# Kernel tuning notes

Measured on AMD Instinct MI355X. Metric: run time of the kernel, lower is better.

## Reference

```python
import jax, jax.numpy as jnp
import numpy as np


def setup_inputs() -> dict:
    key = jax.random.key(0)
    k_xyz, k_w1, k_b1, k_w2, k_b2 = jax.random.split(key, 5)
    B, N = 2, 1024
    D_MODEL, N_HEADS = 128, 8
    HID = D_MODEL // 2
    # Kaiming-ish init scale for the tiny MLP weights
    return {
        "xyz": jax.random.normal(k_xyz, (B, 3, N), dtype=jnp.float32),
        "W1": jax.random.normal(k_w1, (3, HID), dtype=jnp.float32) * (1.0 / np.sqrt(3.0)),
        "b1": jax.random.normal(k_b1, (HID,), dtype=jnp.float32) * 0.01,
        "W2": jax.random.normal(k_w2, (HID, N_HEADS), dtype=jnp.float32) * (1.0 / np.sqrt(HID)),
        "b2": jax.random.normal(k_b2, (N_HEADS,), dtype=jnp.float32) * 0.01,
    }


def reference(xyz, W1, b1, W2, b2):
    # xyz: [B, 3, N] -> [B, N, 3]
    pts = jnp.transpose(xyz, (0, 2, 1))
    # pairwise relative positions: rel[b, i, j, :] = pts[b, j] - pts[b, i]
    # (matches xyz.unsqueeze(1) - xyz.unsqueeze(2) in torch)
    rel = pts[:, None, :, :] - pts[:, :, None, :]          # [B, N, N, 3]
    h = jax.nn.relu(jnp.einsum("bijc,ch->bijh", rel, W1) + b1)  # [B, N, N, HID]
    bias = jnp.einsum("bijh,hk->bijk", h, W2) + b2         # [B, N, N, H]
    # permute(0, 3, 1, 2) -> [B, H, N, N]
    return jnp.transpose(bias, (0, 3, 1, 2))
```

## Files before the change

### kernel.cpp

```cpp
#include <hip/hip_runtime.h>
#include <hip/hip_bf16.h>

#define HID   64
#define NHD   8
#define IT    16
#define WAVES 8
#define JTW   32
#define JT    (WAVES*JTW)

typedef __attribute__((ext_vector_type(8))) short bf16x8;
typedef __attribute__((ext_vector_type(4))) float f32x4;

static __device__ __forceinline__ short f2bf(float f) {
  __hip_bfloat16 h = __float2bfloat16(f);
  short s; __builtin_memcpy(&s, &h, sizeof(s));
  return s;
}

__global__ __launch_bounds__(WAVES * 64, 4) void relposenc_mfma(
    const float* __restrict__ xyz, const float* __restrict__ W1,
    const float* __restrict__ b1,  const float* __restrict__ W2,
    const float* __restrict__ b2,  float* __restrict__ out, int N) {

  __shared__ float sW1b1[4][HID];
  __shared__ float sU[IT][HID];

  const int tid  = threadIdx.x;
  const int wave = tid >> 6;
  const int lane = tid & 63;
  const int col  = lane & 15;
  const int hgrp = lane >> 4;
  const int b    = blockIdx.z;
  const int i0   = blockIdx.y * IT;
  const int j0   = blockIdx.x * JT + wave * JTW;

  const float* xb = xyz + (size_t)b * 3 * N;

  if (tid < 4 * HID) {
    int r = tid >> 6, h = tid & 63;
    sW1b1[r][h] = (r < 3) ? W1[r * HID + h] : b1[h];
  }
  for (int t = tid; t < IT * HID; t += WAVES * 64) {
    int ii = t >> 6, h = t & 63;
    int i  = i0 + ii;
    sU[ii][h] = fmaf(xb[i], W1[h],
                fmaf(xb[N + i], W1[HID + h],
                     xb[2 * N + i] * W1[2 * HID + h]));
  }

  bf16x8 afrag[2];
  #pragma unroll
  for (int kb = 0; kb < 2; ++kb)
    #pragma unroll
    for (int e = 0; e < 8; ++e) {
      int h = kb * 32 + hgrp * 8 + e;
      float w = (col < NHD) ? W2[h * NHD + col] : 0.f;
      afrag[kb][e] = f2bf(w);
    }
  float b2v[4];
  #pragma unroll
  for (int r = 0; r < 4; ++r) b2v[r] = b2[(hgrp * 4 + r) & 7];

  __syncthreads();

  float aj[2][2][8];
  #pragma unroll
  for (int t = 0; t < 2; ++t) {
    int j = j0 + t * 16 + col;
    float x0 = xb[j], x1 = xb[N + j], x2 = xb[2 * N + j];
    #pragma unroll
    for (int kb = 0; kb < 2; ++kb)
      #pragma unroll
      for (int e = 0; e < 8; ++e) {
        int h = kb * 32 + hgrp * 8 + e;
        aj[t][kb][e] = fmaf(x0, sW1b1[0][h],
                       fmaf(x1, sW1b1[1][h],
                       fmaf(x2, sW1b1[2][h], sW1b1[3][h])));
      }
  }

  for (int ii = 0; ii < IT; ++ii) {
    const float4* pu = (const float4*)(&sU[ii][0]);
    float4 u0 = pu[hgrp * 2], u1 = pu[hgrp * 2 + 1];
    float4 u2 = pu[8 + hgrp * 2], u3 = pu[8 + hgrp * 2 + 1];
    float ui[2][8] = {{u0.x,u0.y,u0.z,u0.w, u1.x,u1.y,u1.z,u1.w},
                      {u2.x,u2.y,u2.z,u2.w, u3.x,u3.y,u3.z,u3.w}};
    const int i = i0 + ii;

    #pragma unroll
    for (int t = 0; t < 2; ++t) {
      f32x4 c = {0.f, 0.f, 0.f, 0.f};
      #pragma unroll
      for (int kb = 0; kb < 2; ++kb) {
        bf16x8 bf;
        #pragma unroll
        for (int e = 0; e < 8; ++e) {
          float v = aj[t][kb][e] - ui[kb][e];
          bf[e] = f2bf(v > 0.f ? v : 0.f);
        }
        c = __builtin_amdgcn_mfma_f32_16x16x32_bf16(afrag[kb], bf, c, 0, 0, 0);
      }
      if (lane < 32) {
        size_t jj = (size_t)j0 + t * 16 + col;
        #pragma unroll
        for (int r = 0; r < 4; ++r) {
          int k = hgrp * 4 + r;
          out[(((size_t)(b * NHD + k)) * N + i) * N + jj] = c[r] + b2v[r];
        }
      }
    }
  }
}

extern "C" void kernel_launch(void* const* d_in, const int* in_sizes, int n_in,
                              void* d_out, int out_size, void* d_ws, size_t ws_size,
                              hipStream_t stream) {
  const float* xyz = (const float*)d_in[0];
  const float* W1  = (const float*)d_in[1];
  const float* b1  = (const float*)d_in[2];
  const float* W2  = (const float*)d_in[3];
  const float* b2  = (const float*)d_in[4];
  float* out = (float*)d_out;

  const long long in0 = in_sizes[0];
  const int N = (int)((3LL * (long long)out_size) / (8LL * in0));
  const int B = (int)(in0 / (3LL * N));

  dim3 grid(N / JT, N / IT, B);
  relposenc_mfma<<<grid, WAVES * 64, 0, stream>>>(xyz, W1, b1, W2, b2, out, N);
}
```

Before: 24.31 us.

## Pack two j-tiles into one MFMA accumulator and use nontemporal stores

```diff
diff --git a/kernel.cpp b/kernel.cpp
--- a/kernel.cpp
+++ b/kernel.cpp
@@ -17,7 +17,7 @@
   return s;
 }
 
-__global__ __launch_bounds__(WAVES * 64, 4) void relposenc_mfma(
+__global__ __launch_bounds__(WAVES * 64, 4) void relposenc_mfma3(
     const float* __restrict__ xyz, const float* __restrict__ W1,
     const float* __restrict__ b1,  const float* __restrict__ W2,
     const float* __restrict__ b2,  float* __restrict__ out, int N) {
@@ -48,18 +48,18 @@
                      xb[2 * N + i] * W1[2 * HID + h]));
   }
 
-  bf16x8 afrag[2];
+  bf16x8 aLo[2], aHi[2];
   #pragma unroll
   for (int kb = 0; kb < 2; ++kb)
     #pragma unroll
     for (int e = 0; e < 8; ++e) {
       int h = kb * 32 + hgrp * 8 + e;
-      float w = (col < NHD) ? W2[h * NHD + col] : 0.f;
-      afrag[kb][e] = f2bf(w);
+      aLo[kb][e] = f2bf((col < NHD)  ? W2[h * NHD + col]        : 0.f);
+      aHi[kb][e] = f2bf((col >= NHD) ? W2[h * NHD + (col - 8)]  : 0.f);
     }
   float b2v[4];
   #pragma unroll
-  for (int r = 0; r < 4; ++r) b2v[r] = b2[(hgrp * 4 + r) & 7];
+  for (int r = 0; r < 4; ++r) b2v[r] = b2[((hgrp & 1) << 2) + r];
 
   __syncthreads();
 
@@ -79,35 +79,46 @@
       }
   }
 
+  const size_t jj = (size_t)j0 + col + ((size_t)(lane >> 5) << 4);
+  const int kbase = (hgrp & 1) << 2;
+  float* outp = out + ((size_t)(b * NHD + kbase) * N) * N + jj;
+  const size_t planeStride = (size_t)N * N;
+
+  const float4* pu = (const float4*)(&sU[0][0]);
+  float4 nu0 = pu[hgrp * 2],     nu1 = pu[hgrp * 2 + 1];
+  float4 nu2 = pu[8 + hgrp * 2], nu3 = pu[8 + hgrp * 2 + 1];
+
   for (int ii = 0; ii < IT; ++ii) {
-    const float4* pu = (const float4*)(&sU[ii][0]);
-    float4 u0 = pu[hgrp * 2], u1 = pu[hgrp * 2 + 1];
-    float4 u2 = pu[8 + hgrp * 2], u3 = pu[8 + hgrp * 2 + 1];
+    float4 u0 = nu0, u1 = nu1, u2 = nu2, u3 = nu3;
+    if (ii + 1 < IT) {
+      const float4* pn = (const float4*)(&sU[ii + 1][0]);
+      nu0 = pn[hgrp * 2];     nu1 = pn[hgrp * 2 + 1];
+      nu2 = pn[8 + hgrp * 2]; nu3 = pn[8 + hgrp * 2 + 1];
+    }
     float ui[2][8] = {{u0.x,u0.y,u0.z,u0.w, u1.x,u1.y,u1.z,u1.w},
                       {u2.x,u2.y,u2.z,u2.w, u3.x,u3.y,u3.z,u3.w}};
-    const int i = i0 + ii;
 
+    bf16x8 bf[2][2];
     #pragma unroll
-    for (int t = 0; t < 2; ++t) {
-      f32x4 c = {0.f, 0.f, 0.f, 0.f};
+    for (int t = 0; t < 2; ++t)
       #pragma unroll
-      for (int kb = 0; kb < 2; ++kb) {
-        bf16x8 bf;
+      for (int kb = 0; kb < 2; ++kb)
         #pragma unroll
         for (int e = 0; e < 8; ++e) {
           float v = aj[t][kb][e] - ui[kb][e];
-          bf[e] = f2bf(v > 0.f ? v : 0.f);
+          bf[t][kb][e] = f2bf(v > 0.f ? v : 0.f);
         }
-        c = __builtin_amdgcn_mfma_f32_16x16x32_bf16(afrag[kb], bf, c, 0, 0, 0);
-      }
-      if (lane < 32) {
-        size_t jj = (size_t)j0 + t * 16 + col;
-        #pragma unroll
-        for (int r = 0; r < 4; ++r) {
-          int k = hgrp * 4 + r;
-          out[(((size_t)(b * NHD + k)) * N + i) * N + jj] = c[r] + b2v[r];
-        }
-      }
+
+    f32x4 c = {0.f, 0.f, 0.f, 0.f};
+    c = __builtin_amdgcn_mfma_f32_16x16x32_bf16(aLo[0], bf[0][0], c, 0, 0, 0);
+    c = __builtin_amdgcn_mfma_f32_16x16x32_bf16(aLo[1], bf[0][1], c, 0, 0, 0);
+    c = __builtin_amdgcn_mfma_f32_16x16x32_bf16(aHi[0], bf[1][0], c, 0, 0, 0);
+    c = __builtin_amdgcn_mfma_f32_16x16x32_bf16(aHi[1], bf[1][1], c, 0, 0, 0);
+
+    float* p = outp + (size_t)(i0 + ii) * N;
+    #pragma unroll
+    for (int r = 0; r < 4; ++r) {
+      __builtin_nontemporal_store(c[r] + b2v[r], p + (size_t)r * planeStride);
     }
   }
 }
@@ -127,5 +138,5 @@
   const int B = (int)(in0 / (3LL * N));
 
   dim3 grid(N / JT, N / IT, B);
-  relposenc_mfma<<<grid, WAVES * 64, 0, stream>>>(xyz, W1, b1, W2, b2, out, N);
+  relposenc_mfma3<<<grid, WAVES * 64, 0, stream>>>(xyz, W1, b1, W2, b2, out, N);
 }
```

New measurement: 28.42 us. 1.17x slower.
